# Kernel tuning notes

Measured on AMD Instinct MI355X. Metric: run time of the kernel, lower is better.

The kernel has to match this reference:

```python
import jax, jax.numpy as jnp
import numpy as np
import math

B, T, D, H, E, K = 2, 2048, 1024, 16, 8, 2
F = 4 * D
HD = D // H
EPS = 1e-5


def layer_norm(x, w):
    mu = jnp.mean(x, axis=-1, keepdims=True)
    var = jnp.mean(jnp.square(x - mu), axis=-1, keepdims=True)
    return (x - mu) / jnp.sqrt(var + EPS) * w


def setup_inputs() -> dict:
    key = jax.random.key(0)
    ks = jax.random.split(key, 8)
    s = 0.02
    return {
        "x": jax.random.normal(ks[0], (B, T, D), dtype=jnp.float32),
        "ln1_w": jnp.ones((D,), dtype=jnp.float32),
        "wqkv": jax.random.normal(ks[1], (D, 3 * D), dtype=jnp.float32) * s,
        "wproj": jax.random.normal(ks[2], (D, D), dtype=jnp.float32) * s,
        "ln2_w": jnp.ones((D,), dtype=jnp.float32),
        "router_w": jax.random.normal(ks[3], (D, E), dtype=jnp.float32) * s,
        "w1": jax.random.normal(ks[4], (E, D, F), dtype=jnp.float32) * s,
        "w2": jax.random.normal(ks[5], (E, F, D), dtype=jnp.float32) * s,
    }


def reference(x, ln1_w, wqkv, wproj, ln2_w, router_w, w1, w2):
    # --- self-attention (causal, no bias, dropout=0, eval mode) ---
    h = layer_norm(x, ln1_w)
    qkv = h @ wqkv  # [B,T,3D]
    q, k, v = jnp.split(qkv, 3, axis=-1)
    q = q.reshape(B, T, H, HD).transpose(0, 2, 1, 3)  # [B,H,T,HD]
    k = k.reshape(B, T, H, HD).transpose(0, 2, 1, 3)
    v = v.reshape(B, T, H, HD).transpose(0, 2, 1, 3)
    scores = jnp.einsum("bhqd,bhkd->bhqk", q, k) / math.sqrt(HD)
    causal = jnp.tril(jnp.ones((T, T), dtype=bool))
    scores = jnp.where(causal, scores, jnp.float32(-1e9))
    attn = jax.nn.softmax(scores, axis=-1)
    o = jnp.einsum("bhqk,bhkd->bhqd", attn, v)
    o = o.transpose(0, 2, 1, 3).reshape(B, T, D) @ wproj
    x = x + o

    # --- pre-MoE norm (note: residual for MoE uses ln2 output, per source) ---
    x = layer_norm(x, ln2_w)

    # --- router (eval mode: top-k of softmax probs) ---
    logits = x @ router_w  # [B,T,E]
    probs = jax.nn.softmax(logits, axis=-1)
    _, topi = jax.lax.top_k(probs, K)  # [B,T,K]
    mask = jax.nn.one_hot(topi, E, dtype=probs.dtype).sum(axis=-2)  # [B,T,E]
    rp = probs * mask
    rp = rp / jnp.sum(rp, axis=-1, keepdims=True)  # normalize=True, top_k>1

    # --- experts: dense-equivalent of gather/MLP/scatter (zero-prob tokens contribute 0) ---
    hh = jax.nn.gelu(jnp.einsum("btd,edf->ebtf", x, w1), approximate=False)
    eo = jnp.einsum("ebtf,efd->ebtd", hh, w2)
    next_states = jnp.einsum("bte,ebtd->btd", rp, eo)
    return x + next_states
```

## Files before the change

### kernel.cpp

```cpp
#include <hip/hip_runtime.h>
#include <hip/hip_bf16.h>
#include <math.h>

#define Bv 2
#define Tv 2048
#define Dv 1024
#define Hv 16
#define Ev 8
#define Kv 2
#define Fv 4096
#define HDv 64
#define NT 4096
#define MAXTILES 72

typedef __attribute__((ext_vector_type(8))) short short8;
typedef __attribute__((ext_vector_type(4))) float f32x4;

__device__ __forceinline__ short f2bf(float f) {
  unsigned u = __builtin_bit_cast(unsigned, f);
  u += 0x7fffu + ((u >> 16) & 1u);
  return (short)(u >> 16);
}
__device__ __forceinline__ float bf2f(short s) {
  unsigned u = ((unsigned)(unsigned short)s) << 16;
  return __builtin_bit_cast(float, u);
}
__device__ __forceinline__ float wredsum(float s) {
  #pragma unroll
  for (int off = 32; off; off >>= 1) s += __shfl_down(s, off, 64);
  return s;
}
__device__ __forceinline__ void gl_lds16(const short* g, short* l) {
  __builtin_amdgcn_global_load_lds(
      (const __attribute__((address_space(1))) unsigned int*)g,
      (__attribute__((address_space(3))) unsigned int*)l, 16, 0, 0);
}

__global__ __launch_bounds__(256) void transpose_cvt(const float* __restrict__ in,
                                                     short* __restrict__ out,
                                                     int Kd, int Nd) {
  __shared__ float tile[64][65];
  const float* inb = in + (size_t)blockIdx.z * Kd * Nd;
  short* outb = out + (size_t)blockIdx.z * Kd * Nd;
  const int k0 = blockIdx.x * 64, n0 = blockIdx.y * 64;
  const int rr = threadIdx.x >> 4, cc = (threadIdx.x & 15) * 4;
  #pragma unroll
  for (int i = 0; i < 4; i++) {
    int r = rr + i * 16;
    f32x4 v = *(const f32x4*)(inb + (size_t)(k0 + r) * Nd + n0 + cc);
    tile[r][cc] = v[0]; tile[r][cc + 1] = v[1];
    tile[r][cc + 2] = v[2]; tile[r][cc + 3] = v[3];
  }
  __syncthreads();
  #pragma unroll
  for (int i = 0; i < 2; i++) {
    int e = threadIdx.x + i * 256;
    int n = e >> 3, c = (e & 7) * 8;
    short8 v;
    #pragma unroll
    for (int j = 0; j < 8; j++) v[j] = f2bf(tile[c + j][n]);
    *(short8*)(outb + (size_t)(n0 + n) * Kd + k0 + c) = v;
  }
}

__global__ __launch_bounds__(256) void vtrans_kernel(const short* __restrict__ qkv,
                                                     short* __restrict__ vT) {
  __shared__ short tile[64][72];
  const int t0 = blockIdx.x * 64;
  const int bh = blockIdx.y;
  const int b = bh >> 4, h = bh & 15;
  #pragma unroll
  for (int i = 0; i < 2; i++) {
    int e = threadIdx.x + i * 256;
    int r = e >> 3, c = (e & 7) * 8;
    short8 v = *(const short8*)(qkv + (size_t)(b * Tv + t0 + r) * 3072 + 2048 + h * 64 + c);
    *(short8*)(&tile[r][c]) = v;
  }
  __syncthreads();
  #pragma unroll
  for (int i = 0; i < 2; i++) {
    int e = threadIdx.x + i * 256;
    int d = e >> 3, c = (e & 7) * 8;
    short8 v;
    #pragma unroll
    for (int j = 0; j < 8; j++) v[j] = tile[c + j][d];
    *(short8*)(vT + ((size_t)bh * 64 + d) * Tv + t0 + c) = v;
  }
}

__global__ __launch_bounds__(256) void ln_kernel(const float* __restrict__ in,
                                                 const float* __restrict__ w,
                                                 float* __restrict__ outf,
                                                 short* __restrict__ outb) {
  int t = blockIdx.x;
  int tid = threadIdx.x;
  const float* row = in + (size_t)t * Dv;
  float v[4]; float s = 0.f;
  #pragma unroll
  for (int i = 0; i < 4; i++) { v[i] = row[tid + i * 256]; s += v[i]; }
  s = wredsum(s);
  __shared__ float red[4], red2[4];
  int wv = tid >> 6, ln = tid & 63;
  if (ln == 0) red[wv] = s;
  __syncthreads();
  float mu = (red[0] + red[1] + red[2] + red[3]) * (1.f / Dv);
  float vs = 0.f;
  #pragma unroll
  for (int i = 0; i < 4; i++) { float d = v[i] - mu; vs += d * d; }
  vs = wredsum(vs);
  if (ln == 0) red2[wv] = vs;
  __syncthreads();
  float var = (red2[0] + red2[1] + red2[2] + red2[3]) * (1.f / Dv);
  float inv = rsqrtf(var + 1e-5f);
  #pragma unroll
  for (int i = 0; i < 4; i++) {
    int d = tid + i * 256;
    float o = (v[i] - mu) * inv * w[d];
    if (outf) outf[(size_t)t * Dv + d] = o;
    if (outb) outb[(size_t)t * Dv + d] = f2bf(o);
  }
}

enum { EPI_BF16 = 0, EPI_RESID = 1, EPI_GELU = 2 };

template<int EPI, bool MOE, bool INDIRECT, int KC>
__global__ __launch_bounds__(256) void gemm_lds(
    const short* __restrict__ A, const short* __restrict__ Bt,
    short* __restrict__ Cb, float* __restrict__ Cf,
    const float* __restrict__ resid,
    const int* __restrict__ perm, const int* __restrict__ tiles,
    int M, int N) {
  __shared__ short As[128][32];
  __shared__ short Bs[128][32];
  const int nwg = gridDim.x * gridDim.y;
  const int orig = blockIdx.y * gridDim.x + blockIdx.x;
  const int cpx = nwg >> 3;
  const int wgid = (orig & 7) * cpx + (orig >> 3);
  const int mt = wgid % gridDim.x;
  const int npan = wgid / gridDim.x;

  int row0, row_end;
  const short* Bp = Bt;
  if (MOE) {
    int ntile = tiles[0];
    if (mt >= ntile) return;
    int e   = tiles[1 + mt * 3];
    row0    = tiles[2 + mt * 3];
    row_end = tiles[3 + mt * 3];
    Bp = Bt + (size_t)e * KC * N;
  } else {
    row0 = mt * 128; row_end = M;
  }
  const int nbase = npan * 128;
  const int tid = threadIdx.x;
  const int lane = tid & 63;
  const int w = tid >> 6;
  const int wm = (w >> 1) * 64, wn = (w & 1) * 64;
  const int lr = lane & 15, lk = (lane >> 4) * 8;

  const int lrow = lane >> 2, lcol = (lane & 3) * 8;
  const short* asrc[2]; short* adst[2];
  const short* bsrc[2]; short* bdst[2];
  #pragma unroll
  for (int i = 0; i < 2; i++) {
    int grow = row0 + w * 16 + i * 64 + lrow;
    if (MOE) grow = min(grow, row_end - 1);
    int arow = INDIRECT ? perm[grow] : grow;
    asrc[i] = A + (size_t)arow * KC + lcol;
    adst[i] = &As[w * 16 + i * 64][0];
    bsrc[i] = Bp + (size_t)(nbase + w * 16 + i * 64 + lrow) * KC + lcol;
    bdst[i] = &Bs[w * 16 + i * 64][0];
  }

  f32x4 acc[4][4];
  #pragma unroll
  for (int m = 0; m < 4; m++)
    #pragma unroll
    for (int n = 0; n < 4; n++) acc[m][n] = (f32x4)0.0f;

  #pragma unroll 1
  for (int k0 = 0; k0 < KC; k0 += 128) {
    #pragma unroll
    for (int j = 0; j < 4; j++) {
      #pragma unroll
      for (int i = 0; i < 2; i++) {
        gl_lds16(asrc[i] + k0 + j * 32, adst[i]);
        gl_lds16(bsrc[i] + k0 + j * 32, bdst[i]);
      }
      __syncthreads();
      short8 af[4], bfr[4];
      #pragma unroll
      for (int m = 0; m < 4; m++) af[m] = *(const short8*)(&As[wm + m * 16 + lr][lk]);
      #pragma unroll
      for (int n = 0; n < 4; n++) bfr[n] = *(const short8*)(&Bs[wn + n * 16 + lr][lk]);
      #pragma unroll
      for (int m = 0; m < 4; m++)
        #pragma unroll
        for (int n = 0; n < 4; n++)
          acc[m][n] = __builtin_amdgcn_mfma_f32_16x16x32_bf16(af[m], bfr[n], acc[m][n], 0, 0, 0);
      __syncthreads();
    }
  }
  #pragma unroll
  for (int m = 0; m < 4; m++) {
    #pragma unroll
    for (int n = 0; n < 4; n++) {
      #pragma unroll
      for (int r = 0; r < 4; r++) {
        int row = row0 + wm + m * 16 + (lane >> 4) * 4 + r;
        if (MOE && row >= row_end) continue;
        int col = nbase + wn + n * 16 + lr;
        float v = acc[m][n][r];
        size_t idx = (size_t)row * N + col;
        if (EPI == EPI_BF16) {
          Cb[idx] = f2bf(v);
        } else if (EPI == EPI_RESID) {
          Cf[idx] = v + resid[idx];
        } else if (EPI == EPI_GELU) {
          float g = 0.5f * v * (1.0f + erff(v * 0.70710678118f));
          Cb[idx] = f2bf(g);
        } else {
          Cb[idx] = f2bf(v);
        }
      }
    }
  }
}

#define SCL2E 0.18033688011112042f

__global__ __launch_bounds__(256) void attn_kernel(const short* __restrict__ qkv,
                                                   const short* __restrict__ vT,
                                                   short* __restrict__ o) {
  const int qbase = ((int)gridDim.x - 1 - (int)blockIdx.x) * 64;
  const int bh = blockIdx.y;
  const int b = bh >> 4, h = bh & 15;
  const int w = threadIdx.x >> 6, lane = threadIdx.x & 63;
  const int lr = lane & 15, lkg = lane >> 4, lk = lkg * 8;
  const size_t rs = 3 * Dv;

  __shared__ short Ks[64][72];
  __shared__ short Vs[64][72];
  __shared__ short Ps[4][16][72];

  short8 qf[2];
  {
    size_t qrow = (size_t)(b * Tv + qbase + w * 16 + lr) * rs + h * 64;
    qf[0] = *(const short8*)(qkv + qrow + lk);
    qf[1] = *(const short8*)(qkv + qrow + 32 + lk);
  }
  f32x4 oacc[4];
  #pragma unroll
  for (int n = 0; n < 4; n++) oacc[n] = (f32x4)0.0f;
  float mrow[4] = {-INFINITY, -INFINITY, -INFINITY, -INFINITY};
  float lrow4[4] = {0.f, 0.f, 0.f, 0.f};

  const short* kbase = qkv + (size_t)b * Tv * rs + Dv + h * 64;
  const short* vbase = vT + (size_t)bh * 64 * Tv;

  for (int kv0 = 0; kv0 < qbase + 64; kv0 += 64) {
    #pragma unroll
    for (int i = 0; i < 2; i++) {
      int e = threadIdx.x + i * 256;
      int r = e >> 3, c = (e & 7) * 8;
      short8 kval = *(const short8*)(kbase + (size_t)(kv0 + r) * rs + c);
      *(short8*)(&Ks[r][c]) = kval;
      short8 vval = *(const short8*)(vbase + (size_t)r * Tv + kv0 + c);
      *(short8*)(&Vs[r][c]) = vval;
    }
    __syncthreads();
    f32x4 s[4];
    #pragma unroll
    for (int n = 0; n < 4; n++) {
      s[n] = (f32x4)0.0f;
      short8 kf0 = *(const short8*)(&Ks[n * 16 + lr][lk]);
      short8 kf1 = *(const short8*)(&Ks[n * 16 + lr][32 + lk]);
      s[n] = __builtin_amdgcn_mfma_f32_16x16x32_bf16(qf[0], kf0, s[n], 0, 0, 0);
      s[n] = __builtin_amdgcn_mfma_f32_16x16x32_bf16(qf[1], kf1, s[n], 0, 0, 0);
    }
    if (kv0 < qbase) {
      #pragma unroll
      for (int n = 0; n < 4; n++)
        #pragma unroll
        for (int r = 0; r < 4; r++) s[n][r] *= SCL2E;
    } else {
      #pragma unroll
      for (int n = 0; n < 4; n++)
        #pragma unroll
        for (int r = 0; r < 4; r++) {
          int tq = qbase + w * 16 + lkg * 4 + r;
          int tk = kv0 + n * 16 + lr;
          s[n][r] = (tk > tq) ? -1e30f : s[n][r] * SCL2E;
        }
    }
    float scr[4];
    #pragma unroll
    for (int r = 0; r < 4; r++) {
      float m = fmaxf(fmaxf(s[0][r], s[1][r]), fmaxf(s[2][r], s[3][r]));
      #pragma unroll
      for (int off = 8; off; off >>= 1) m = fmaxf(m, __shfl_xor(m, off, 64));
      float mnew = fmaxf(mrow[r], m);
      float sc = exp2f(mrow[r] - mnew);
      float rsum = 0.f;
      #pragma unroll
      for (int n = 0; n < 4; n++) { float p = exp2f(s[n][r] - mnew); s[n][r] = p; rsum += p; }
      #pragma unroll
      for (int off = 8; off; off >>= 1) rsum += __shfl_xor(rsum, off, 64);
      lrow4[r] = lrow4[r] * sc + rsum;
      mrow[r] = mnew;
      scr[r] = sc;
    }
    #pragma unroll
    for (int n = 0; n < 4; n++)
      #pragma unroll
      for (int r = 0; r < 4; r++) Ps[w][lkg * 4 + r][n * 16 + lr] = f2bf(s[n][r]);
    #pragma unroll
    for (int n = 0; n < 4; n++)
      #pragma unroll
      for (int r = 0; r < 4; r++) oacc[n][r] *= scr[r];
    __syncthreads();
    #pragma unroll
    for (int n2 = 0; n2 < 4; n2++) {
      short8 pf0 = *(const short8*)(&Ps[w][lr][lk]);
      short8 pf1 = *(const short8*)(&Ps[w][lr][32 + lk]);
      short8 vf0 = *(const short8*)(&Vs[n2 * 16 + lr][lk]);
      short8 vf1 = *(const short8*)(&Vs[n2 * 16 + lr][32 + lk]);
      oacc[n2] = __builtin_amdgcn_mfma_f32_16x16x32_bf16(pf0, vf0, oacc[n2], 0, 0, 0);
      oacc[n2] = __builtin_amdgcn_mfma_f32_16x16x32_bf16(pf1, vf1, oacc[n2], 0, 0, 0);
    }
    __syncthreads();
  }
  float rinv[4];
  #pragma unroll
  for (int r = 0; r < 4; r++) rinv[r] = 1.0f / lrow4[r];
  #pragma unroll
  for (int n2 = 0; n2 < 4; n2++)
    #pragma unroll
    for (int r = 0; r < 4; r++) {
      int tq = qbase + w * 16 + lkg * 4 + r;
      float v = oacc[n2][r] * rinv[r];
      o[(size_t)(b * Tv + tq) * Dv + h * 64 + n2 * 16 + lr] = f2bf(v);
    }
}

__global__ __launch_bounds__(256) void router_kernel(const float* __restrict__ x2f,
                                                     const float* __restrict__ rw,
                                                     int* __restrict__ topi,
                                                     float* __restrict__ topp) {
  int w = threadIdx.x >> 6, lane = threadIdx.x & 63;
  int t = blockIdx.x * 4 + w;
  const float* row = x2f + (size_t)t * Dv;
  float acc[8];
  #pragma unroll
  for (int e = 0; e < 8; e++) acc[e] = 0.f;
  for (int i = 0; i < 16; i++) {
    int d = lane + i * 64;
    float xv = row[d];
    const float* rwp = rw + (size_t)d * 8;
    #pragma unroll
    for (int e = 0; e < 8; e++) acc[e] += xv * rwp[e];
  }
  #pragma unroll
  for (int e = 0; e < 8; e++) acc[e] = wredsum(acc[e]);
  if (lane == 0) {
    float mx = acc[0];
    #pragma unroll
    for (int e = 1; e < 8; e++) mx = fmaxf(mx, acc[e]);
    float p[8]; float se = 0.f;
    #pragma unroll
    for (int e = 0; e < 8; e++) { p[e] = expf(acc[e] - mx); se += p[e]; }
    #pragma unroll
    for (int e = 0; e < 8; e++) p[e] /= se;
    int i1 = 0; float p1 = p[0];
    #pragma unroll
    for (int e = 1; e < 8; e++) if (p[e] > p1) { p1 = p[e]; i1 = e; }
    float pm = p[i1]; p[i1] = -1.f;
    int i2 = 0; float p2 = p[0];
    #pragma unroll
    for (int e = 1; e < 8; e++) if (p[e] > p2) { p2 = p[e]; i2 = e; }
    float sum = pm + p2;
    topi[t * 2] = i1; topi[t * 2 + 1] = i2;
    topp[t * 2] = pm / sum; topp[t * 2 + 1] = p2 / sum;
  }
}

__global__ void bucket_count(const int* __restrict__ topi, int* __restrict__ offsets,
                             int* __restrict__ cursor) {
  __shared__ int cnt[8];
  if (threadIdx.x < 8) { cnt[threadIdx.x] = 0; cursor[threadIdx.x] = 0; }
  __syncthreads();
  for (int i = threadIdx.x; i < NT * 2; i += 256) atomicAdd(&cnt[topi[i]], 1);
  __syncthreads();
  if (threadIdx.x == 0) {
    int s = 0;
    for (int e = 0; e < 8; e++) { offsets[e] = s; s += cnt[e]; }
    offsets[8] = s;
  }
}
__global__ void bucket_scatter(const int* __restrict__ topi, const int* __restrict__ offsets,
                               int* __restrict__ cursor, int* __restrict__ perm,
                               int* __restrict__ row_of) {
  int i = blockIdx.x * 256 + threadIdx.x;
  if (i >= NT * 2) return;
  int e = topi[i];
  int slot = atomicAdd(&cursor[e], 1);
  int r = offsets[e] + slot;
  perm[r] = i >> 1;
  row_of[i] = r;
}
__global__ void tile_build(const int* __restrict__ offsets, int* __restrict__ tiles) {
  if (threadIdx.x == 0 && blockIdx.x == 0) {
    int nt = 0;
    for (int e = 0; e < 8; e++) {
      int r0 = offsets[e], r1 = offsets[e + 1];
      for (int m = r0; m < r1; m += 128) {
        tiles[1 + nt * 3] = e; tiles[2 + nt * 3] = m; tiles[3 + nt * 3] = r1; nt++;
      }
    }
    tiles[0] = nt;
  }
}

__global__ __launch_bounds__(256) void final_kernel(float* __restrict__ out,
                                                    const short* __restrict__ eout,
                                                    const int* __restrict__ row_of,
                                                    const float* __restrict__ topp) {
  int t = blockIdx.x; int tid = threadIdx.x;
  int r0 = row_of[t * 2], r1 = row_of[t * 2 + 1];
  float p0 = topp[t * 2], p1 = topp[t * 2 + 1];
  #pragma unroll
  for (int i = 0; i < 4; i++) {
    int d = tid + i * 256;
    out[(size_t)t * Dv + d] += p0 * bf2f(eout[(size_t)r0 * Dv + d])
                             + p1 * bf2f(eout[(size_t)r1 * Dv + d]);
  }
}

extern "C" void kernel_launch(void* const* d_in, const int* in_sizes, int n_in,
                              void* d_out, int out_size, void* d_ws, size_t ws_size,
                              hipStream_t stream) {
  const float* x        = (const float*)d_in[0];
  const float* ln1_w    = (const float*)d_in[1];
  const float* wqkv     = (const float*)d_in[2];
  const float* wproj    = (const float*)d_in[3];
  const float* ln2_w    = (const float*)d_in[4];
  const float* router_w = (const float*)d_in[5];
  const float* w1       = (const float*)d_in[6];
  const float* w2       = (const float*)d_in[7];
  float* out = (float*)d_out;
  char* ws = (char*)d_ws;

  size_t off = 0;
  short* wqkvT  = (short*)(ws + off); off += (size_t)3 * Dv * Dv * 2;
  short* wprojT = (short*)(ws + off); off += (size_t)Dv * Dv * 2;
  short* w1T    = (short*)(ws + off); off += (size_t)Ev * Dv * Fv * 2;
  short* w2T    = (short*)(ws + off); off += (size_t)Ev * Fv * Dv * 2;
  char* reg1 = ws + off; off += (size_t)NT * Dv * 2;
  short* hln1 = (short*)reg1;
  short* ob   = (short*)reg1;
  short* x2b  = (short*)reg1;
  char* reg2 = ws + off; off += (size_t)NT * 3 * Dv * 2;
  short* qkvb = (short*)reg2;
  float* xres = (float*)reg2;
  char* reg3 = ws + off; off += (size_t)NT * 2 * Fv * 2;
  short* vT = (short*)reg3;
  short* Hb = (short*)reg3;
  short* eout = (short*)(ws + off); off += (size_t)NT * 2 * Dv * 2;
  int*   topi = (int*)(ws + off);   off += NT * 2 * 4;
  float* topp = (float*)(ws + off); off += NT * 2 * 4;
  int*   offs = (int*)(ws + off);   off += 64;
  int*   cur  = (int*)(ws + off);   off += 64;
  int*   perm = (int*)(ws + off);   off += NT * 2 * 4;
  int*   rowof= (int*)(ws + off);   off += NT * 2 * 4;
  int*   tiles= (int*)(ws + off);   off += 1024;

  transpose_cvt<<<dim3(Dv / 64, 3 * Dv / 64, 1), 256, 0, stream>>>(wqkv, wqkvT, Dv, 3 * Dv);
  transpose_cvt<<<dim3(Dv / 64, Dv / 64, 1), 256, 0, stream>>>(wproj, wprojT, Dv, Dv);
  transpose_cvt<<<dim3(Dv / 64, Fv / 64, Ev), 256, 0, stream>>>(w1, w1T, Dv, Fv);
  transpose_cvt<<<dim3(Fv / 64, Dv / 64, Ev), 256, 0, stream>>>(w2, w2T, Fv, Dv);

  ln_kernel<<<NT, 256, 0, stream>>>(x, ln1_w, nullptr, hln1);
  gemm_lds<EPI_BF16, false, false, Dv><<<dim3(NT / 128, 3 * Dv / 128), 256, 0, stream>>>(
      hln1, wqkvT, qkvb, nullptr, nullptr, nullptr, nullptr, NT, 3 * Dv);
  vtrans_kernel<<<dim3(Tv / 64, Bv * Hv), 256, 0, stream>>>(qkvb, vT);
  attn_kernel<<<dim3(Tv / 64, Bv * Hv), 256, 0, stream>>>(qkvb, vT, ob);
  gemm_lds<EPI_RESID, false, false, Dv><<<dim3(NT / 128, Dv / 128), 256, 0, stream>>>(
      ob, wprojT, nullptr, xres, x, nullptr, nullptr, NT, Dv);
  ln_kernel<<<NT, 256, 0, stream>>>(xres, ln2_w, out, x2b);
  router_kernel<<<NT / 4, 256, 0, stream>>>(out, router_w, topi, topp);
  bucket_count<<<1, 256, 0, stream>>>(topi, offs, cur);
  bucket_scatter<<<NT * 2 / 256, 256, 0, stream>>>(topi, offs, cur, perm, rowof);
  tile_build<<<1, 1, 0, stream>>>(offs, tiles);
  gemm_lds<EPI_GELU, true, true, Dv><<<dim3(MAXTILES, Fv / 128), 256, 0, stream>>>(
      x2b, w1T, Hb, nullptr, nullptr, perm, tiles, 0, Fv);
  gemm_lds<EPI_BF16, true, false, Fv><<<dim3(MAXTILES, Dv / 128), 256, 0, stream>>>(
      Hb, w2T, eout, nullptr, nullptr, nullptr, tiles, 0, Dv);
  final_kernel<<<NT, 256, 0, stream>>>(out, eout, rowof, topp);
}
```

Baseline: 619.7 us.

## Double-buffer LDS tiles in GEMM to overlap global loads with MFMA

Splits the shared-memory A/B tiles into two buffers. The next K-slice is loaded directly into LDS while the current one is computed, using explicit vmcnt waits and barriers instead of syncing after each load. The goal is to hide global-memory latency behind the MFMA work in the attention and MoE GEMMs. It doubles LDS use per block, which may reduce occupancy, and it depends on the hand-written waitcnt counts being correct.

Measured after the change: 625.2 us, median of 2. No clear change (+0.9%).

```diff
diff --git a/kernel.cpp b/kernel.cpp
--- a/kernel.cpp
+++ b/kernel.cpp
@@ -130,8 +130,8 @@
     const float* __restrict__ resid,
     const int* __restrict__ perm, const int* __restrict__ tiles,
     int M, int N) {
-  __shared__ short As[128][32];
-  __shared__ short Bs[128][32];
+  __shared__ short As[2][128][32];
+  __shared__ short Bs[2][128][32];
   const int nwg = gridDim.x * gridDim.y;
   const int orig = blockIdx.y * gridDim.x + blockIdx.x;
   const int cpx = nwg >> 3;
@@ -159,18 +159,23 @@
   const int lr = lane & 15, lk = (lane >> 4) * 8;
 
   const int lrow = lane >> 2, lcol = (lane & 3) * 8;
-  const short* asrc[2]; short* adst[2];
-  const short* bsrc[2]; short* bdst[2];
+  const short* asrc[2];
+  const short* bsrc[2];
   #pragma unroll
   for (int i = 0; i < 2; i++) {
     int grow = row0 + w * 16 + i * 64 + lrow;
     if (MOE) grow = min(grow, row_end - 1);
     int arow = INDIRECT ? perm[grow] : grow;
     asrc[i] = A + (size_t)arow * KC + lcol;
-    adst[i] = &As[w * 16 + i * 64][0];
     bsrc[i] = Bp + (size_t)(nbase + w * 16 + i * 64 + lrow) * KC + lcol;
-    bdst[i] = &Bs[w * 16 + i * 64][0];
-  }
+  }
+
+  auto STAGE = [&](int b, int k0) {
+    gl_lds16(asrc[0] + k0, &As[b][w * 16][0]);
+    gl_lds16(bsrc[0] + k0, &Bs[b][w * 16][0]);
+    gl_lds16(asrc[1] + k0, &As[b][w * 16 + 64][0]);
+    gl_lds16(bsrc[1] + k0, &Bs[b][w * 16 + 64][0]);
+  };
 
   f32x4 acc[4][4];
   #pragma unroll
@@ -178,28 +183,41 @@
     #pragma unroll
     for (int n = 0; n < 4; n++) acc[m][n] = (f32x4)0.0f;
 
+  auto COMPUTE = [&](int b) {
+    short8 af[4], bfr[4];
+    #pragma unroll
+    for (int m = 0; m < 4; m++) af[m] = *(const short8*)(&As[b][wm + m * 16 + lr][lk]);
+    #pragma unroll
+    for (int n = 0; n < 4; n++) bfr[n] = *(const short8*)(&Bs[b][wn + n * 16 + lr][lk]);
+    #pragma unroll
+    for (int m = 0; m < 4; m++)
+      #pragma unroll
+      for (int n = 0; n < 4; n++)
+        acc[m][n] = __builtin_amdgcn_mfma_f32_16x16x32_bf16(af[m], bfr[n], acc[m][n], 0, 0, 0);
+  };
+
+  constexpr int KT = KC / 32;
+  STAGE(0, 0);
   #pragma unroll 1
-  for (int k0 = 0; k0 < KC; k0 += 128) {
-    #pragma unroll
-    for (int j = 0; j < 4; j++) {
-      #pragma unroll
-      for (int i = 0; i < 2; i++) {
-        gl_lds16(asrc[i] + k0 + j * 32, adst[i]);
-        gl_lds16(bsrc[i] + k0 + j * 32, bdst[i]);
-      }
-      __syncthreads();
-      short8 af[4], bfr[4];
-      #pragma unroll
-      for (int m = 0; m < 4; m++) af[m] = *(const short8*)(&As[wm + m * 16 + lr][lk]);
-      #pragma unroll
-      for (int n = 0; n < 4; n++) bfr[n] = *(const short8*)(&Bs[wn + n * 16 + lr][lk]);
-      #pragma unroll
-      for (int m = 0; m < 4; m++)
-        #pragma unroll
-        for (int n = 0; n < 4; n++)
-          acc[m][n] = __builtin_amdgcn_mfma_f32_16x16x32_bf16(af[m], bfr[n], acc[m][n], 0, 0, 0);
-      __syncthreads();
-    }
+  for (int kt = 0; kt < KT; kt += 2) {
+    STAGE(1, (kt + 1) * 32);
+    asm volatile("s_waitcnt vmcnt(4)" ::: "memory");
+    __builtin_amdgcn_s_barrier();
+    __builtin_amdgcn_sched_barrier(0);
+    COMPUTE(0);
+    __builtin_amdgcn_sched_barrier(0);
+    __builtin_amdgcn_s_barrier();
+    if (kt + 2 < KT) {
+      STAGE(0, (kt + 2) * 32);
+      asm volatile("s_waitcnt vmcnt(4)" ::: "memory");
+    } else {
+      asm volatile("s_waitcnt vmcnt(0)" ::: "memory");
+    }
+    __builtin_amdgcn_s_barrier();
+    __builtin_amdgcn_sched_barrier(0);
+    COMPUTE(1);
+    __builtin_amdgcn_sched_barrier(0);
+    __builtin_amdgcn_s_barrier();
   }
   #pragma unroll
   for (int m = 0; m < 4; m++) {
```

## Triple-buffer GEMM LDS tiles and register-prefetch attention K/V blocks

Applied to the files above, without the earlier changes.

The GEMM main loop now keeps three LDS stages and issues async global-to-LDS loads two K-steps ahead, using vmcnt waits and one barrier per step instead of two syncthreads per 32-wide slice. The attention kernel prefetches the next K/V block into registers while the current block computes, and raises wave priority around the MFMA sections. This aims to hide global load latency behind matrix math. In exchange it triples GEMM LDS use (less occupancy headroom) and adds an extra barrier per attention iteration.

Measured after the change: 855.1 us. 38.0% more time.

```diff
diff --git a/kernel.cpp b/kernel.cpp
--- a/kernel.cpp
+++ b/kernel.cpp
@@ -130,8 +130,8 @@
     const float* __restrict__ resid,
     const int* __restrict__ perm, const int* __restrict__ tiles,
     int M, int N) {
-  __shared__ short As[128][32];
-  __shared__ short Bs[128][32];
+  __shared__ short As[3][128][32];
+  __shared__ short Bs[3][128][32];
   const int nwg = gridDim.x * gridDim.y;
   const int orig = blockIdx.y * gridDim.x + blockIdx.x;
   const int cpx = nwg >> 3;
@@ -159,18 +159,23 @@
   const int lr = lane & 15, lk = (lane >> 4) * 8;
 
   const int lrow = lane >> 2, lcol = (lane & 3) * 8;
-  const short* asrc[2]; short* adst[2];
-  const short* bsrc[2]; short* bdst[2];
+  const short* asrc[2];
+  const short* bsrc[2];
   #pragma unroll
   for (int i = 0; i < 2; i++) {
     int grow = row0 + w * 16 + i * 64 + lrow;
     if (MOE) grow = min(grow, row_end - 1);
     int arow = INDIRECT ? perm[grow] : grow;
     asrc[i] = A + (size_t)arow * KC + lcol;
-    adst[i] = &As[w * 16 + i * 64][0];
     bsrc[i] = Bp + (size_t)(nbase + w * 16 + i * 64 + lrow) * KC + lcol;
-    bdst[i] = &Bs[w * 16 + i * 64][0];
-  }
+  }
+
+  auto STAGE = [&](short (*Ad)[32], short (*Bd)[32], int k0) {
+    gl_lds16(asrc[0] + k0, &Ad[w * 16][0]);
+    gl_lds16(bsrc[0] + k0, &Bd[w * 16][0]);
+    gl_lds16(asrc[1] + k0, &Ad[w * 16 + 64][0]);
+    gl_lds16(bsrc[1] + k0, &Bd[w * 16 + 64][0]);
+  };
 
   f32x4 acc[4][4];
   #pragma unroll
@@ -178,28 +183,41 @@
     #pragma unroll
     for (int n = 0; n < 4; n++) acc[m][n] = (f32x4)0.0f;
 
+  auto COMPUTE = [&](short (*Ab)[32], short (*Bb)[32]) {
+    short8 af[4], bfr[4];
+    #pragma unroll
+    for (int m = 0; m < 4; m++) af[m] = *(const short8*)(&Ab[wm + m * 16 + lr][lk]);
+    #pragma unroll
+    for (int n = 0; n < 4; n++) bfr[n] = *(const short8*)(&Bb[wn + n * 16 + lr][lk]);
+    #pragma unroll
+    for (int m = 0; m < 4; m++)
+      #pragma unroll
+      for (int n = 0; n < 4; n++)
+        acc[m][n] = __builtin_amdgcn_mfma_f32_16x16x32_bf16(af[m], bfr[n], acc[m][n], 0, 0, 0);
+  };
+
+  constexpr int KT = KC / 32;
+  STAGE(As[0], Bs[0], 0);
+  STAGE(As[1], Bs[1], 32);
+  asm volatile("s_waitcnt vmcnt(4)" ::: "memory");
+  __builtin_amdgcn_s_barrier();
+
+  short (*Ar)[32] = As[0]; short (*Br)[32] = Bs[0];
+  short (*An)[32] = As[1]; short (*Bn)[32] = Bs[1];
+  short (*Aw)[32] = As[2]; short (*Bw)[32] = Bs[2];
   #pragma unroll 1
-  for (int k0 = 0; k0 < KC; k0 += 128) {
-    #pragma unroll
-    for (int j = 0; j < 4; j++) {
-      #pragma unroll
-      for (int i = 0; i < 2; i++) {
-        gl_lds16(asrc[i] + k0 + j * 32, adst[i]);
-        gl_lds16(bsrc[i] + k0 + j * 32, bdst[i]);
-      }
-      __syncthreads();
-      short8 af[4], bfr[4];
-      #pragma unroll
-      for (int m = 0; m < 4; m++) af[m] = *(const short8*)(&As[wm + m * 16 + lr][lk]);
-      #pragma unroll
-      for (int n = 0; n < 4; n++) bfr[n] = *(const short8*)(&Bs[wn + n * 16 + lr][lk]);
-      #pragma unroll
-      for (int m = 0; m < 4; m++)
-        #pragma unroll
-        for (int n = 0; n < 4; n++)
-          acc[m][n] = __builtin_amdgcn_mfma_f32_16x16x32_bf16(af[m], bfr[n], acc[m][n], 0, 0, 0);
-      __syncthreads();
-    }
+  for (int t = 0; t < KT; ++t) {
+    if (t + 2 < KT) {
+      STAGE(Aw, Bw, (t + 2) * 32);
+      COMPUTE(Ar, Br);
+      asm volatile("s_waitcnt vmcnt(4)" ::: "memory");
+    } else {
+      COMPUTE(Ar, Br);
+      asm volatile("s_waitcnt vmcnt(0)" ::: "memory");
+    }
+    __builtin_amdgcn_s_barrier();
+    short (*ta)[32] = Ar; Ar = An; An = Aw; Aw = ta;
+    short (*tb)[32] = Br; Br = Bn; Bn = Bw; Bw = tb;
   }
   #pragma unroll
   for (int m = 0; m < 4; m++) {
@@ -258,18 +276,35 @@
   const short* kbase = qkv + (size_t)b * Tv * rs + Dv + h * 64;
   const short* vbase = vT + (size_t)bh * 64 * Tv;
 
-  for (int kv0 = 0; kv0 < qbase + 64; kv0 += 64) {
+  short8 kreg[2], vreg[2];
+  auto LOADKV = [&](int kv0) {
     #pragma unroll
     for (int i = 0; i < 2; i++) {
       int e = threadIdx.x + i * 256;
       int r = e >> 3, c = (e & 7) * 8;
-      short8 kval = *(const short8*)(kbase + (size_t)(kv0 + r) * rs + c);
-      *(short8*)(&Ks[r][c]) = kval;
-      short8 vval = *(const short8*)(vbase + (size_t)r * Tv + kv0 + c);
-      *(short8*)(&Vs[r][c]) = vval;
-    }
-    __syncthreads();
+      kreg[i] = *(const short8*)(kbase + (size_t)(kv0 + r) * rs + c);
+      vreg[i] = *(const short8*)(vbase + (size_t)r * Tv + kv0 + c);
+    }
+  };
+  auto WRITEKV = [&]() {
+    #pragma unroll
+    for (int i = 0; i < 2; i++) {
+      int e = threadIdx.x + i * 256;
+      int r = e >> 3, c = (e & 7) * 8;
+      *(short8*)(&Ks[r][c]) = kreg[i];
+      *(short8*)(&Vs[r][c]) = vreg[i];
+    }
+  };
+
+  const int kvend = qbase + 64;
+  LOADKV(0);
+  WRITEKV();
+  __syncthreads();
+  for (int kv0 = 0; kv0 < kvend; kv0 += 64) {
+    const bool more = (kv0 + 64) < kvend;
+    if (more) LOADKV(kv0 + 64);
     f32x4 s[4];
+    __builtin_amdgcn_s_setprio(1);
     #pragma unroll
     for (int n = 0; n < 4; n++) {
       s[n] = (f32x4)0.0f;
@@ -278,6 +313,7 @@
       s[n] = __builtin_amdgcn_mfma_f32_16x16x32_bf16(qf[0], kf0, s[n], 0, 0, 0);
       s[n] = __builtin_amdgcn_mfma_f32_16x16x32_bf16(qf[1], kf1, s[n], 0, 0, 0);
     }
+    __builtin_amdgcn_s_setprio(0);
     if (kv0 < qbase) {
       #pragma unroll
       for (int n = 0; n < 4; n++)
@@ -319,6 +355,7 @@
       #pragma unroll
       for (int r = 0; r < 4; r++) oacc[n][r] *= scr[r];
     __syncthreads();
+    __builtin_amdgcn_s_setprio(1);
     #pragma unroll
     for (int n2 = 0; n2 < 4; n2++) {
       short8 pf0 = *(const short8*)(&Ps[w][lr][lk]);
@@ -328,7 +365,12 @@
       oacc[n2] = __builtin_amdgcn_mfma_f32_16x16x32_bf16(pf0, vf0, oacc[n2], 0, 0, 0);
       oacc[n2] = __builtin_amdgcn_mfma_f32_16x16x32_bf16(pf1, vf1, oacc[n2], 0, 0, 0);
     }
+    __builtin_amdgcn_s_setprio(0);
     __syncthreads();
+    if (more) {
+      WRITEKV();
+      __syncthreads();
+    }
   }
   float rinv[4];
   #pragma unroll
```

## Prefetch next K/V tile into registers during attention compute, add MFMA priority

Applied to the files above, without the earlier changes.

The attention loop now issues global loads for the next K/V tile into registers before computing on the current tile, then writes them to shared memory after the PV MFMAs. This hides global-load latency behind the QK and PV work. It also raises wave priority around the MFMA blocks with s_setprio. The cost is extra registers per thread and an extra barrier per iteration.

After: 642.7 us. 3.7% more time.

```diff
diff --git a/kernel.cpp b/kernel.cpp
--- a/kernel.cpp
+++ b/kernel.cpp
@@ -258,18 +258,35 @@
   const short* kbase = qkv + (size_t)b * Tv * rs + Dv + h * 64;
   const short* vbase = vT + (size_t)bh * 64 * Tv;
 
-  for (int kv0 = 0; kv0 < qbase + 64; kv0 += 64) {
+  short8 kreg[2], vreg[2];
+  auto LOADKV = [&](int kv0) {
     #pragma unroll
     for (int i = 0; i < 2; i++) {
       int e = threadIdx.x + i * 256;
       int r = e >> 3, c = (e & 7) * 8;
-      short8 kval = *(const short8*)(kbase + (size_t)(kv0 + r) * rs + c);
-      *(short8*)(&Ks[r][c]) = kval;
-      short8 vval = *(const short8*)(vbase + (size_t)r * Tv + kv0 + c);
-      *(short8*)(&Vs[r][c]) = vval;
-    }
-    __syncthreads();
+      kreg[i] = *(const short8*)(kbase + (size_t)(kv0 + r) * rs + c);
+      vreg[i] = *(const short8*)(vbase + (size_t)r * Tv + kv0 + c);
+    }
+  };
+  auto WRITEKV = [&]() {
+    #pragma unroll
+    for (int i = 0; i < 2; i++) {
+      int e = threadIdx.x + i * 256;
+      int r = e >> 3, c = (e & 7) * 8;
+      *(short8*)(&Ks[r][c]) = kreg[i];
+      *(short8*)(&Vs[r][c]) = vreg[i];
+    }
+  };
+
+  const int kvend = qbase + 64;
+  LOADKV(0);
+  WRITEKV();
+  __syncthreads();
+  for (int kv0 = 0; kv0 < kvend; kv0 += 64) {
+    const bool more = (kv0 + 64) < kvend;
+    if (more) LOADKV(kv0 + 64);
     f32x4 s[4];
+    __builtin_amdgcn_s_setprio(1);
     #pragma unroll
     for (int n = 0; n < 4; n++) {
       s[n] = (f32x4)0.0f;
@@ -278,6 +295,7 @@
       s[n] = __builtin_amdgcn_mfma_f32_16x16x32_bf16(qf[0], kf0, s[n], 0, 0, 0);
       s[n] = __builtin_amdgcn_mfma_f32_16x16x32_bf16(qf[1], kf1, s[n], 0, 0, 0);
     }
+    __builtin_amdgcn_s_setprio(0);
     if (kv0 < qbase) {
       #pragma unroll
       for (int n = 0; n < 4; n++)
@@ -319,6 +337,7 @@
       #pragma unroll
       for (int r = 0; r < 4; r++) oacc[n][r] *= scr[r];
     __syncthreads();
+    __builtin_amdgcn_s_setprio(1);
     #pragma unroll
     for (int n2 = 0; n2 < 4; n2++) {
       short8 pf0 = *(const short8*)(&Ps[w][lr][lk]);
@@ -328,7 +347,12 @@
       oacc[n2] = __builtin_amdgcn_mfma_f32_16x16x32_bf16(pf0, vf0, oacc[n2], 0, 0, 0);
       oacc[n2] = __builtin_amdgcn_mfma_f32_16x16x32_bf16(pf1, vf1, oacc[n2], 0, 0, 0);
     }
+    __builtin_amdgcn_s_setprio(0);
     __syncthreads();
+    if (more) {
+      WRITEKV();
+      __syncthreads();
+    }
   }
   float rinv[4];
   #pragma unroll
```
